# Kernel tuning notes

Hardware: AMD Instinct MI355X
Metric: run time of the kernel (lower is better)

Reference implementation:

```python
import jax, jax.numpy as jnp
import numpy as np

N_NODES = 50000
N_EDGES = 400000
D = 300          # num_features == hidden_units
L = 5            # num_layers
C = 128          # num_outputs
NG = 256         # graphs per batch
BN_EPS = 1e-5


def setup_inputs() -> dict:
    key = jax.random.key(0)
    ks = jax.random.split(key, 16)
    x = jax.random.normal(ks[0], (N_NODES, D), dtype=jnp.float32)
    edge_index = jax.random.randint(ks[1], (2, N_EDGES), 0, N_NODES, dtype=jnp.int64)
    batch = jnp.sort(jax.random.randint(ks[2], (N_NODES,), 0, NG, dtype=jnp.int64))
    s = 1.0 / np.sqrt(D)
    # Stacked per-layer GINConv MLP params: Linear -> BN -> ReLU -> Linear, then outer BN
    mlp_W1 = jax.random.uniform(ks[3], (L, D, D), jnp.float32, -s, s)
    mlp_b1 = jax.random.uniform(ks[4], (L, D), jnp.float32, -s, s)
    mlp_g1 = jnp.ones((L, D), jnp.float32)
    mlp_be1 = jnp.zeros((L, D), jnp.float32)
    mlp_W2 = jax.random.uniform(ks[5], (L, D, D), jnp.float32, -s, s)
    mlp_b2 = jax.random.uniform(ks[6], (L, D), jnp.float32, -s, s)
    bn_g = jnp.ones((L, D), jnp.float32)
    bn_b = jnp.zeros((L, D), jnp.float32)
    # num_layers+1 readout heads (num_features == hidden_units so all [D, C])
    fc_W = jax.random.uniform(ks[7], (L + 1, D, C), jnp.float32, -s, s)
    fc_b = jax.random.uniform(ks[8], (L + 1, C), jnp.float32, -s, s)
    return dict(x=x, edge_index=edge_index, batch=batch,
                mlp_W1=mlp_W1, mlp_b1=mlp_b1, mlp_g1=mlp_g1, mlp_be1=mlp_be1,
                mlp_W2=mlp_W2, mlp_b2=mlp_b2, bn_g=bn_g, bn_b=bn_b,
                fc_W=fc_W, fc_b=fc_b)


def _bn(h, gamma, beta):
    # BatchNorm1d in training mode: biased batch stats over the node dim
    mu = h.mean(axis=0)
    var = h.var(axis=0)
    return (h - mu) * jax.lax.rsqrt(var + BN_EPS) * gamma + beta


def reference(x, edge_index, batch, mlp_W1, mlp_b1, mlp_g1, mlp_be1,
              mlp_W2, mlp_b2, bn_g, bn_b, fc_W, fc_b):
    src, dst = edge_index[0], edge_index[1]
    n = x.shape[0]
    outs = [x]
    h = x
    for i in range(L):
        # GINConv (eps=0): MLP(x + sum_{j in N(i)} x_j), scatter-add over edges
        agg = jax.ops.segment_sum(h[src], dst, num_segments=n)
        z = h + agg
        z = z @ mlp_W1[i] + mlp_b1[i]
        z = jax.nn.relu(_bn(z, mlp_g1[i], mlp_be1[i]))
        z = z @ mlp_W2[i] + mlp_b2[i]
        h = jax.nn.relu(_bn(z, bn_g[i], bn_b[i]))  # outer BN + ReLU
        outs.append(h)
    # global mean pool per graph, then per-depth linear heads summed (dropout off in eval)
    counts = jax.ops.segment_sum(jnp.ones((n,), x.dtype), batch, num_segments=NG)
    inv = 1.0 / jnp.maximum(counts, 1.0)
    out = jnp.zeros((NG, C), x.dtype)
    for i, hi in enumerate(outs):
        pooled = jax.ops.segment_sum(hi, batch, num_segments=NG) * inv[:, None]
        out = out + (pooled @ fc_W[i] + fc_b[i])
    return out
```

## Files before the change

### kernel.cpp

```cpp
#include <hip/hip_runtime.h>

#define D 300
#define KP 320
#define NPAD 50048
#define NT128 391
#define TPB 2
#define GB 196
#define WSTRIDE 328
#define NGR 256
#define NL 5
#define NC 128
#define BN_EPS 1e-5f

typedef __attribute__((ext_vector_type(8))) short bf16x8;
typedef __attribute__((ext_vector_type(4))) float f32x4;
typedef unsigned short u16;

__device__ __forceinline__ void atomAdd(float* p, float v) { unsafeAtomicAdd(p, v); }

__device__ __forceinline__ short f2bf(float f) {
    union { float f; unsigned u; } v; v.f = f;
    unsigned r = v.u + 0x7fffu + ((v.u >> 16) & 1u);
    return (short)(r >> 16);
}
__device__ __forceinline__ float bf2f(short s) {
    union { unsigned u; float f; } v;
    v.u = ((unsigned)(u16)s) << 16;
    return v.f;
}
__device__ __forceinline__ unsigned cvtpk(float lo, float hi) {
    unsigned r;
    asm("v_cvt_pk_bf16_f32 %0, %1, %2" : "=v"(r) : "v"(lo), "v"(hi));
    return r;
}
template<int C>
__device__ __forceinline__ float rs_add(float v) {
    int x = __builtin_amdgcn_update_dpp(0, __float_as_int(v), C, 0xF, 0xF, true);
    return v + __int_as_float(x);
}
__device__ __forceinline__ float red16(float v) {
    v = rs_add<0x111>(v);
    v = rs_add<0x112>(v);
    v = rs_add<0x114>(v);
    v = rs_add<0x118>(v);
    return v;
}

__global__ void offsets_kernel(const int* __restrict__ batch, int* __restrict__ off, int N) {
    int g = threadIdx.x;
    if (g > NGR) return;
    int lo = 0, hi = N;
    while (lo < hi) {
        int mid = (lo + hi) >> 1;
        if (batch[mid] < g) lo = mid + 1; else hi = mid;
    }
    off[g] = lo;
}

__global__ __launch_bounds__(256)
void deg_kernel(const int* __restrict__ ei, int* __restrict__ deg, int E) {
    int e = blockIdx.x * 256 + threadIdx.x;
    if (e < E) atomicAdd(&deg[ei[E + e]], 1);
}

__global__ __launch_bounds__(256)
void degpart_kernel(const int* __restrict__ deg, int* __restrict__ part, int N) {
    int i = blockIdx.x * 256 + threadIdx.x;
    int v = (i < N) ? deg[i] : 0;
    #pragma unroll
    for (int o = 1; o < 64; o <<= 1) v += __shfl_xor(v, o);
    __shared__ int ws[4];
    if ((threadIdx.x & 63) == 0) ws[threadIdx.x >> 6] = v;
    __syncthreads();
    if (threadIdx.x == 0) part[blockIdx.x] = ws[0] + ws[1] + ws[2] + ws[3];
}

__global__ __launch_bounds__(256)
void partscan_kernel(int* __restrict__ part, int nb) {
    __shared__ int buf[256];
    int t = threadIdx.x;
    int v = (t < nb) ? part[t] : 0;
    buf[t] = v;
    __syncthreads();
    for (int o = 1; o < 256; o <<= 1) {
        int u = (t >= o) ? buf[t - o] : 0;
        __syncthreads();
        buf[t] += u;
        __syncthreads();
    }
    if (t < nb) part[t] = (t == 0) ? 0 : buf[t - 1];
}

__global__ __launch_bounds__(256)
void rowptr_kernel(const int* __restrict__ deg, const int* __restrict__ part,
                   int* __restrict__ rowptr, int N, int E) {
    __shared__ int buf[256];
    int b = blockIdx.x, t = threadIdx.x;
    int i = b * 256 + t;
    int v = (i < N) ? deg[i] : 0;
    buf[t] = v;
    __syncthreads();
    for (int o = 1; o < 256; o <<= 1) {
        int u = (t >= o) ? buf[t - o] : 0;
        __syncthreads();
        buf[t] += u;
        __syncthreads();
    }
    if (i < N) rowptr[i] = part[b] + buf[t] - v;
    if (b == 0 && t == 0) rowptr[N] = E;
}

__global__ __launch_bounds__(256)
void fill_kernel(const int* __restrict__ ei, const int* __restrict__ rowptr,
                 int* __restrict__ cursor, int* __restrict__ col, int E) {
    int e = blockIdx.x * 256 + threadIdx.x;
    if (e >= E) return;
    int src = ei[e];
    int dst = ei[E + e];
    int pos = atomicAdd(&cursor[dst], 1);
    col[rowptr[dst] + pos] = src;
}

__global__ __launch_bounds__(256)
void wcvt_kernel(const float* __restrict__ W1, const float* __restrict__ W2,
                 u16* __restrict__ Wt) {
    int idx = blockIdx.x * 256 + threadIdx.x;
    if (idx >= 10 * KP * 80) return;
    int n4 = idx % 80;
    int k = (idx / 80) % KP;
    int mat = idx / (80 * KP);
    const float* Wsrc = (mat < NL) ? (W1 + (size_t)mat * D * D) : (W2 + (size_t)(mat - NL) * D * D);
    float4 w = make_float4(0.f, 0.f, 0.f, 0.f);
    if (k < D && n4 < 75) w = *(const float4*)(Wsrc + (size_t)k * D + n4 * 4);
    size_t base = ((size_t)mat * 320 + n4 * 4) * KP + k;
    Wt[base]          = (u16)f2bf(w.x);
    Wt[base + KP]     = (u16)f2bf(w.y);
    Wt[base + 2 * KP] = (u16)f2bf(w.z);
    Wt[base + 3 * KP] = (u16)f2bf(w.w);
}

__global__ __launch_bounds__(256)
void xcvt_kernel(const float* __restrict__ x, u16* __restrict__ xbf, int N) {
    int idx = blockIdx.x * 256 + threadIdx.x;
    if (idx >= NPAD * 40) return;
    int row = idx / 40;
    int c8 = (idx - row * 40) * 8;
    short o[8];
    #pragma unroll
    for (int i = 0; i < 8; ++i) {
        int c = c8 + i;
        float f = (row < N && c < D) ? x[(size_t)row * D + c] : 0.f;
        o[i] = f2bf(f);
    }
    *(bf16x8*)(xbf + (size_t)row * KP + c8) = *(bf16x8*)o;
}

template<bool APPLY>
__global__ __launch_bounds__(256)
void gather_kernel(const u16* __restrict__ H, u16* __restrict__ Z,
                   const int* __restrict__ rowptr, const int* __restrict__ col,
                   const float* __restrict__ scsh, int N) {
    int idx = blockIdx.x * 256 + threadIdx.x;
    if (idx >= N * 40) return;
    int node = idx / 40;
    int c8 = (idx - node * 40) * 8;
    float sc[8], sh[8];
    if (APPLY) {
        #pragma unroll
        for (int i = 0; i < 8; ++i) { sc[i] = scsh[c8 + i]; sh[i] = scsh[KP + c8 + i]; }
    }
    int s = rowptr[node], e = rowptr[node + 1];
    bf16x8 v = *(const bf16x8*)(H + (size_t)node * KP + c8);
    float acc[8];
    #pragma unroll
    for (int i = 0; i < 8; ++i) {
        float f = bf2f(v[i]);
        acc[i] = APPLY ? fmaxf(fmaf(f, sc[i], sh[i]), 0.f) : f;
    }
    int j = s;
    for (; j + 2 <= e; j += 2) {
        int s0 = col[j], s1 = col[j + 1];
        bf16x8 w0 = *(const bf16x8*)(H + (size_t)s0 * KP + c8);
        bf16x8 w1 = *(const bf16x8*)(H + (size_t)s1 * KP + c8);
        #pragma unroll
        for (int i = 0; i < 8; ++i) {
            float f0 = bf2f(w0[i]);
            float f1 = bf2f(w1[i]);
            acc[i] += APPLY ? fmaxf(fmaf(f0, sc[i], sh[i]), 0.f) : f0;
            acc[i] += APPLY ? fmaxf(fmaf(f1, sc[i], sh[i]), 0.f) : f1;
        }
    }
    if (j < e) {
        int s0 = col[j];
        bf16x8 w0 = *(const bf16x8*)(H + (size_t)s0 * KP + c8);
        #pragma unroll
        for (int i = 0; i < 8; ++i) {
            float f0 = bf2f(w0[i]);
            acc[i] += APPLY ? fmaxf(fmaf(f0, sc[i], sh[i]), 0.f) : f0;
        }
    }
    short o[8];
    #pragma unroll
    for (int i = 0; i < 8; ++i) o[i] = f2bf(acc[i]);
    *(bf16x8*)(Z + (size_t)node * KP + c8) = *(bf16x8*)o;
}

template<bool APPLY>
__global__ __launch_bounds__(320)
void pool_kernel(const u16* __restrict__ H, const int* __restrict__ off,
                 const float* __restrict__ scsh, float* __restrict__ pooled_l) {
    __shared__ float red[8][KP];
    int t = threadIdx.x;
    int g = blockIdx.x;
    int rq = t / 40;
    int c8 = (t - rq * 40) * 8;
    float sc[8], sh[8];
    if (APPLY) {
        #pragma unroll
        for (int i = 0; i < 8; ++i) { sc[i] = scsh[c8 + i]; sh[i] = scsh[KP + c8 + i]; }
    }
    int r0 = off[g], r1 = off[g + 1];
    float a[8] = {};
    for (int r = r0 + rq; r < r1; r += 8) {
        bf16x8 v = *(const bf16x8*)(H + (size_t)r * KP + c8);
        #pragma unroll
        for (int i = 0; i < 8; ++i) {
            float f = bf2f(v[i]);
            a[i] += APPLY ? fmaxf(fmaf(f, sc[i], sh[i]), 0.f) : f;
        }
    }
    #pragma unroll
    for (int i = 0; i < 8; ++i) red[rq][c8 + i] = a[i];
    __syncthreads();
    int c = t;
    if (c < D) {
        float s = 0.f;
        #pragma unroll
        for (int j = 0; j < 8; ++j) s += red[j][c];
        pooled_l[g * D + c] = s;
    }
}

template<bool APPLY>
__global__ __launch_bounds__(256, 3)
void mfma_gemm_kernel(const u16* __restrict__ Abf, const u16* __restrict__ Wt,
                      const float* __restrict__ bias, const float* __restrict__ scsh,
                      u16* __restrict__ Cbf, float* __restrict__ stats, int Nreal) {
    __shared__ u16 Ws[80 * WSTRIDE];
    __shared__ float lsum[80], lsq[80];
    const int tid = threadIdx.x;
    const int nBase = blockIdx.y * 80;
    const int wave = tid >> 6, lane = tid & 63;
    const int quad = lane >> 4, l16 = lane & 15;

    const int tile0 = blockIdx.x * TPB;
    const u16* pA = Abf + (size_t)(tile0 * 128 + wave * 16 + l16) * KP + quad * 8;
    bf16x8 a[2][10];
    #pragma unroll
    for (int kc = 0; kc < 10; ++kc) {
        a[0][kc] = *(const bf16x8*)(pA + kc * 32);
        a[1][kc] = *(const bf16x8*)(pA + (size_t)64 * KP + kc * 32);
    }
    __builtin_amdgcn_sched_group_barrier(0x020, 20, 0);

    {
        const u16* src = Wt + (size_t)nBase * KP;
        for (int unit = tid; unit < 80 * 40; unit += 256) {
            int n = unit / 40, kg = unit - n * 40;
            int kc = kg >> 2, q = kg & 3;
            *(bf16x8*)&Ws[n * WSTRIDE + kc * 32 + ((q ^ (n & 3)) << 3)] =
                *(const bf16x8*)(src + (size_t)n * KP + kg * 8);
        }
    }
    if (tid < 80) { lsum[tid] = 0.f; lsq[tid] = 0.f; }
    __syncthreads();

    int wb[5];
    #pragma unroll
    for (int nt = 0; nt < 5; ++nt)
        wb[nt] = (nt * 16 + l16) * WSTRIDE + ((quad ^ (l16 & 3)) << 3);

    const size_t adv = (tile0 + 1 < NT128) ? (size_t)128 * KP : 0;

    #pragma unroll
    for (int t = 0; t < TPB; ++t) {
        const int tile = tile0 + t;

        if (APPLY) {
            #pragma unroll
            for (int kc = 0; kc < 10; ++kc) {
                const float* sp = scsh + kc * 32 + quad * 8;
                float4 s0 = *(const float4*)sp;
                float4 s1 = *(const float4*)(sp + 4);
                float4 h0 = *(const float4*)(sp + KP);
                float4 h1 = *(const float4*)(sp + KP + 4);
                float sc[8] = {s0.x, s0.y, s0.z, s0.w, s1.x, s1.y, s1.z, s1.w};
                float sh[8] = {h0.x, h0.y, h0.z, h0.w, h1.x, h1.y, h1.z, h1.w};
                #pragma unroll
                for (int g = 0; g < 2; ++g) {
                    float f[8];
                    #pragma unroll
                    for (int i = 0; i < 8; ++i)
                        f[i] = fmaxf(fmaf(bf2f(a[g][kc][i]), sc[i], sh[i]), 0.f);
                    union { unsigned u[4]; bf16x8 v; } o;
                    o.u[0] = cvtpk(f[0], f[1]);
                    o.u[1] = cvtpk(f[2], f[3]);
                    o.u[2] = cvtpk(f[4], f[5]);
                    o.u[3] = cvtpk(f[6], f[7]);
                    a[g][kc] = o.v;
                }
            }
        }

        f32x4 acc[2][5] = {};
        __builtin_amdgcn_s_setprio(1);
        #pragma unroll
        for (int kc = 0; kc < 10; ++kc) {
            #pragma unroll
            for (int nt = 0; nt < 5; ++nt) {
                bf16x8 b = *(const bf16x8*)&Ws[wb[nt] + kc * 32];
                acc[0][nt] = __builtin_amdgcn_mfma_f32_16x16x32_bf16(b, a[0][kc], acc[0][nt], 0, 0, 0);
                acc[1][nt] = __builtin_amdgcn_mfma_f32_16x16x32_bf16(b, a[1][kc], acc[1][nt], 0, 0, 0);
            }
            if (t == 0) {
                a[0][kc] = *(const bf16x8*)(pA + adv + kc * 32);
                a[1][kc] = *(const bf16x8*)(pA + adv + (size_t)64 * KP + kc * 32);
            }
            __builtin_amdgcn_sched_group_barrier(0x100, 5, 0);
            __builtin_amdgcn_sched_group_barrier(0x008, 10, 0);
            if (t == 0)
                __builtin_amdgcn_sched_group_barrier(0x020, 2, 0);
        }
        __builtin_amdgcn_s_setprio(0);

        if (tile < NT128) {
            const int r0g = tile * 128 + wave * 16 + l16;
            const bool ok0 = r0g < Nreal, ok1 = (r0g + 64) < Nreal;
            u16* crow0 = Cbf + (size_t)r0g * KP + nBase + quad * 4;
            u16* crow1 = crow0 + (size_t)64 * KP;
            #pragma unroll
            for (int nt = 0; nt < 5; ++nt) {
                const int c0 = nBase + nt * 16 + quad * 4;
                float bia[4], msk[4];
                if (c0 + 3 < D) {
                    float4 b4 = *(const float4*)(bias + c0);
                    bia[0] = b4.x; bia[1] = b4.y; bia[2] = b4.z; bia[3] = b4.w;
                    msk[0] = msk[1] = msk[2] = msk[3] = 1.f;
                } else {
                    #pragma unroll
                    for (int r = 0; r < 4; ++r) {
                        bool vld = (c0 + r) < D;
                        msk[r] = vld ? 1.f : 0.f;
                        bia[r] = vld ? bias[c0 + r] : 0.f;
                    }
                }
                float v0[4], v1[4];
                #pragma unroll
                for (int r = 0; r < 4; ++r) {
                    v0[r] = (acc[0][nt][r] + bia[r]) * msk[r];
                    v1[r] = (acc[1][nt][r] + bia[r]) * msk[r];
                }
                uint2 w0, w1;
                w0.x = cvtpk(v0[0], v0[1]); w0.y = cvtpk(v0[2], v0[3]);
                w1.x = cvtpk(v1[0], v1[1]); w1.y = cvtpk(v1[2], v1[3]);
                *(uint2*)(crow0 + nt * 16) = w0;
                *(uint2*)(crow1 + nt * 16) = w1;
                #pragma unroll
                for (int r = 0; r < 4; ++r) {
                    float s0 = ok0 ? v0[r] : 0.f;
                    float s1 = ok1 ? v1[r] : 0.f;
                    float sv = red16(s0 + s1);
                    float qv = red16(fmaf(s0, s0, s1 * s1));
                    if (l16 == 15) {
                        atomicAdd(&lsum[nt * 16 + quad * 4 + r], sv);
                        atomicAdd(&lsq [nt * 16 + quad * 4 + r], qv);
                    }
                }
            }
        }
    }
    __syncthreads();
    if (tid < 80) {
        int colg = nBase + tid;
        if (colg < D) {
            atomAdd(&stats[colg], lsum[tid]);
            atomAdd(&stats[KP + colg], lsq[tid]);
        }
    }
}

__global__ void bnfin_kernel(float* __restrict__ sums, const float* __restrict__ g,
                             const float* __restrict__ be, float* __restrict__ scsh, float invN) {
    int c = threadIdx.x;
    if (c >= D) return;
    float mu = sums[c] * invN;
    float var = sums[KP + c] * invN - mu * mu;
    float s = g[c] / sqrtf(var + BN_EPS);
    scsh[c] = s;
    scsh[KP + c] = fmaf(-mu, s, be[c]);
    sums[c] = 0.f;
    sums[KP + c] = 0.f;
}

__global__ __launch_bounds__(128)
void bias_init_kernel(const float* __restrict__ fcb, float* __restrict__ out) {
    int i = blockIdx.x * 128 + threadIdx.x;
    if (i >= NGR * NC) return;
    int c = i & (NC - 1);
    float s = 0.f;
    for (int l = 0; l <= NL; ++l) s += fcb[l * NC + c];
    out[i] = s;
}

__global__ __launch_bounds__(128)
void readout_kernel(const float* __restrict__ pooled, const int* __restrict__ off,
                    const float* __restrict__ fcW, float* __restrict__ out) {
    __shared__ float sp[4][D];
    int c = threadIdx.x;
    int l = blockIdx.y;
    int g0 = blockIdx.x * 4;
    for (int i = c; i < 4 * D; i += 128) {
        int gg = i / D, k = i - gg * D;
        sp[gg][k] = pooled[((size_t)l * NGR + g0 + gg) * D + k];
    }
    __syncthreads();
    float acc[4] = {0.f, 0.f, 0.f, 0.f};
    for (int k = 0; k < D; ++k) {
        float w = fcW[((size_t)l * D + k) * NC + c];
        #pragma unroll
        for (int gg = 0; gg < 4; ++gg) acc[gg] = fmaf(sp[gg][k], w, acc[gg]);
    }
    #pragma unroll
    for (int gg = 0; gg < 4; ++gg) {
        int g = g0 + gg;
        float inv = 1.0f / fmaxf((float)(off[g + 1] - off[g]), 1.0f);
        atomAdd(&out[g * NC + c], acc[gg] * inv);
    }
}

extern "C" void kernel_launch(void* const* d_in, const int* in_sizes, int n_in,
                              void* d_out, int out_size, void* d_ws, size_t ws_size,
                              hipStream_t stream) {
    const float* x       = (const float*)d_in[0];
    const int*   ei      = (const int*)d_in[1];
    const int*   batch   = (const int*)d_in[2];
    const float* W1  = (const float*)d_in[3];
    const float* b1  = (const float*)d_in[4];
    const float* g1  = (const float*)d_in[5];
    const float* be1 = (const float*)d_in[6];
    const float* W2  = (const float*)d_in[7];
    const float* b2  = (const float*)d_in[8];
    const float* bng = (const float*)d_in[9];
    const float* bnb = (const float*)d_in[10];
    const float* fcW = (const float*)d_in[11];
    const float* fcb = (const float*)d_in[12];
    float* out = (float*)d_out;

    const int N = in_sizes[0] / D;
    const int E = in_sizes[1] / 2;
    const int nb = (N + 255) / 256;

    u16* xbf  = (u16*)d_ws;
    u16* bufA = xbf + (size_t)NPAD * KP;
    u16* bufB = bufA + (size_t)NPAD * KP;
    u16* Wt   = bufB + (size_t)NPAD * KP;
    float* pooled = (float*)(Wt + (size_t)10 * 320 * KP);
    float* stats  = pooled + (size_t)(NL + 1) * NGR * D;
    float* sc1    = stats + 2 * KP;
    float* sc2    = sc1 + 2 * KP;
    int*   off    = (int*)(sc2 + 2 * KP);
    int*   rowptr = off + NGR + 1;
    int*   cursor = rowptr + N + 1;
    int*   col    = cursor + N;
    int*   part   = col + E;

    hipMemsetAsync(stats, 0, 6 * KP * sizeof(float), stream);
    offsets_kernel<<<1, 320, 0, stream>>>(batch, off, N);
    bias_init_kernel<<<(NGR * NC + 127) / 128, 128, 0, stream>>>(fcb, out);

    hipMemsetAsync(cursor, 0, N * sizeof(int), stream);
    deg_kernel<<<(E + 255) / 256, 256, 0, stream>>>(ei, cursor, E);
    degpart_kernel<<<nb, 256, 0, stream>>>(cursor, part, N);
    partscan_kernel<<<1, 256, 0, stream>>>(part, nb);
    rowptr_kernel<<<nb, 256, 0, stream>>>(cursor, part, rowptr, N, E);
    hipMemsetAsync(cursor, 0, N * sizeof(int), stream);
    fill_kernel<<<(E + 255) / 256, 256, 0, stream>>>(ei, rowptr, cursor, col, E);

    wcvt_kernel<<<(10 * KP * 80 + 255) / 256, 256, 0, stream>>>(W1, W2, Wt);
    xcvt_kernel<<<(NPAD * 40 + 255) / 256, 256, 0, stream>>>(x, xbf, N);

    const dim3 gemm_grid(GB, 4);
    const int nd40 = N * 40;
    float invN = 1.0f / (float)N;
    const size_t WtM = (size_t)320 * KP;

    pool_kernel<false><<<NGR, 320, 0, stream>>>(xbf, off, sc2, pooled);

    u16* g = bufA;
    u16* t = bufB;
    const u16* src = xbf;
    for (int l = 0; l < NL; ++l) {
        if (l == 0)
            gather_kernel<false><<<(nd40 + 255) / 256, 256, 0, stream>>>(src, g, rowptr, col, sc2, N);
        else
            gather_kernel<true><<<(nd40 + 255) / 256, 256, 0, stream>>>(src, g, rowptr, col, sc2, N);
        mfma_gemm_kernel<false><<<gemm_grid, 256, 0, stream>>>(
            g, Wt + (size_t)l * WtM, b1 + l * D, sc1, t, stats, N);
        bnfin_kernel<<<1, 320, 0, stream>>>(stats, g1 + l * D, be1 + l * D, sc1, invN);
        mfma_gemm_kernel<true><<<gemm_grid, 256, 0, stream>>>(
            t, Wt + (size_t)(NL + l) * WtM, b2 + l * D, sc1, g, stats, N);
        bnfin_kernel<<<1, 320, 0, stream>>>(stats, bng + l * D, bnb + l * D, sc2, invN);
        pool_kernel<true><<<NGR, 320, 0, stream>>>(g, off, sc2, pooled + (size_t)(l + 1) * NGR * D);
        src = g;
        u16* tmp = g; g = t; t = tmp;
    }
    readout_kernel<<<dim3(NGR / 4, NL + 1), 128, 0, stream>>>(pooled, off, fcW, out);
}
```

Baseline: 1.011 ms.

## Drop GEMM biases before BN, use one tile per block, partition stat atomics

Removes the bias add and column masking from the GEMM epilogue, since a per-column bias just before training-mode BatchNorm cancels in the mean subtraction. The GEMM goes back to one 128-row tile per block (grid of 391x4) without the software-prefetched second tile. Global BN stat accumulation is spread over 8 partitions keyed on block index to cut atomic contention, and bnfin sums and clears the partitions. Dropping the bias changes stored bf16 values slightly, and padded columns now depend on the zero-padded weights rather than explicit masking.

New measurement: 1.007 ms. About the same (-0.4%).

```diff
diff --git a/kernel.cpp b/kernel.cpp
--- a/kernel.cpp
+++ b/kernel.cpp
@@ -4,12 +4,11 @@
 #define KP 320
 #define NPAD 50048
 #define NT128 391
-#define TPB 2
-#define GB 196
 #define WSTRIDE 328
 #define NGR 256
 #define NL 5
 #define NC 128
+#define SPART 8
 #define BN_EPS 1e-5f
 
 typedef __attribute__((ext_vector_type(8))) short bf16x8;
@@ -244,7 +243,7 @@
 template<bool APPLY>
 __global__ __launch_bounds__(256, 3)
 void mfma_gemm_kernel(const u16* __restrict__ Abf, const u16* __restrict__ Wt,
-                      const float* __restrict__ bias, const float* __restrict__ scsh,
+                      const float* __restrict__ scsh,
                       u16* __restrict__ Cbf, float* __restrict__ stats, int Nreal) {
     __shared__ u16 Ws[80 * WSTRIDE];
     __shared__ float lsum[80], lsq[80];
@@ -252,16 +251,15 @@
     const int nBase = blockIdx.y * 80;
     const int wave = tid >> 6, lane = tid & 63;
     const int quad = lane >> 4, l16 = lane & 15;
-
-    const int tile0 = blockIdx.x * TPB;
-    const u16* pA = Abf + (size_t)(tile0 * 128 + wave * 16 + l16) * KP + quad * 8;
+    const int tile = blockIdx.x;
+
+    const u16* pA = Abf + (size_t)(tile * 128 + wave * 16 + l16) * KP + quad * 8;
     bf16x8 a[2][10];
     #pragma unroll
     for (int kc = 0; kc < 10; ++kc) {
         a[0][kc] = *(const bf16x8*)(pA + kc * 32);
         a[1][kc] = *(const bf16x8*)(pA + (size_t)64 * KP + kc * 32);
     }
-    __builtin_amdgcn_sched_group_barrier(0x020, 20, 0);
 
     {
         const u16* src = Wt + (size_t)nBase * KP;
@@ -273,109 +271,81 @@
         }
     }
     if (tid < 80) { lsum[tid] = 0.f; lsq[tid] = 0.f; }
-    __syncthreads();
+
+    #pragma unroll
+    for (int kc = 0; kc < 10; ++kc) {
+        asm volatile("" : "+v"(a[0][kc]));
+        asm volatile("" : "+v"(a[1][kc]));
+    }
+    __syncthreads();
+
+    if (APPLY) {
+        #pragma unroll
+        for (int kc = 0; kc < 10; ++kc) {
+            const float* sp = scsh + kc * 32 + quad * 8;
+            float4 s0 = *(const float4*)sp;
+            float4 s1 = *(const float4*)(sp + 4);
+            float4 h0 = *(const float4*)(sp + KP);
+            float4 h1 = *(const float4*)(sp + KP + 4);
+            float sc[8] = {s0.x, s0.y, s0.z, s0.w, s1.x, s1.y, s1.z, s1.w};
+            float sh[8] = {h0.x, h0.y, h0.z, h0.w, h1.x, h1.y, h1.z, h1.w};
+            #pragma unroll
+            for (int g = 0; g < 2; ++g) {
+                float f[8];
+                #pragma unroll
+                for (int i = 0; i < 8; ++i)
+                    f[i] = fmaxf(fmaf(bf2f(a[g][kc][i]), sc[i], sh[i]), 0.f);
+                union { unsigned u[4]; bf16x8 v; } o;
+                o.u[0] = cvtpk(f[0], f[1]);
+                o.u[1] = cvtpk(f[2], f[3]);
+                o.u[2] = cvtpk(f[4], f[5]);
+                o.u[3] = cvtpk(f[6], f[7]);
+                a[g][kc] = o.v;
+            }
+        }
+    }
 
     int wb[5];
     #pragma unroll
     for (int nt = 0; nt < 5; ++nt)
         wb[nt] = (nt * 16 + l16) * WSTRIDE + ((quad ^ (l16 & 3)) << 3);
 
-    const size_t adv = (tile0 + 1 < NT128) ? (size_t)128 * KP : 0;
-
-    #pragma unroll
-    for (int t = 0; t < TPB; ++t) {
-        const int tile = tile0 + t;
-
-        if (APPLY) {
-            #pragma unroll
-            for (int kc = 0; kc < 10; ++kc) {
-                const float* sp = scsh + kc * 32 + quad * 8;
-                float4 s0 = *(const float4*)sp;
-                float4 s1 = *(const float4*)(sp + 4);
-                float4 h0 = *(const float4*)(sp + KP);
-                float4 h1 = *(const float4*)(sp + KP + 4);
-                float sc[8] = {s0.x, s0.y, s0.z, s0.w, s1.x, s1.y, s1.z, s1.w};
-                float sh[8] = {h0.x, h0.y, h0.z, h0.w, h1.x, h1.y, h1.z, h1.w};
-                #pragma unroll
-                for (int g = 0; g < 2; ++g) {
-                    float f[8];
-                    #pragma unroll
-                    for (int i = 0; i < 8; ++i)
-                        f[i] = fmaxf(fmaf(bf2f(a[g][kc][i]), sc[i], sh[i]), 0.f);
-                    union { unsigned u[4]; bf16x8 v; } o;
-                    o.u[0] = cvtpk(f[0], f[1]);
-                    o.u[1] = cvtpk(f[2], f[3]);
-                    o.u[2] = cvtpk(f[4], f[5]);
-                    o.u[3] = cvtpk(f[6], f[7]);
-                    a[g][kc] = o.v;
-                }
-            }
-        }
-
-        f32x4 acc[2][5] = {};
-        __builtin_amdgcn_s_setprio(1);
-        #pragma unroll
-        for (int kc = 0; kc < 10; ++kc) {
-            #pragma unroll
-            for (int nt = 0; nt < 5; ++nt) {
-                bf16x8 b = *(const bf16x8*)&Ws[wb[nt] + kc * 32];
-                acc[0][nt] = __builtin_amdgcn_mfma_f32_16x16x32_bf16(b, a[0][kc], acc[0][nt], 0, 0, 0);
-                acc[1][nt] = __builtin_amdgcn_mfma_f32_16x16x32_bf16(b, a[1][kc], acc[1][nt], 0, 0, 0);
-            }
-            if (t == 0) {
-                a[0][kc] = *(const bf16x8*)(pA + adv + kc * 32);
-                a[1][kc] = *(const bf16x8*)(pA + adv + (size_t)64 * KP + kc * 32);
-            }
-            __builtin_amdgcn_sched_group_barrier(0x100, 5, 0);
-            __builtin_amdgcn_sched_group_barrier(0x008, 10, 0);
-            if (t == 0)
-                __builtin_amdgcn_sched_group_barrier(0x020, 2, 0);
-        }
-        __builtin_amdgcn_s_setprio(0);
-
-        if (tile < NT128) {
-            const int r0g = tile * 128 + wave * 16 + l16;
-            const bool ok0 = r0g < Nreal, ok1 = (r0g + 64) < Nreal;
-            u16* crow0 = Cbf + (size_t)r0g * KP + nBase + quad * 4;
-            u16* crow1 = crow0 + (size_t)64 * KP;
-            #pragma unroll
-            for (int nt = 0; nt < 5; ++nt) {
-                const int c0 = nBase + nt * 16 + quad * 4;
-                float bia[4], msk[4];
-                if (c0 + 3 < D) {
-                    float4 b4 = *(const float4*)(bias + c0);
-                    bia[0] = b4.x; bia[1] = b4.y; bia[2] = b4.z; bia[3] = b4.w;
-                    msk[0] = msk[1] = msk[2] = msk[3] = 1.f;
-                } else {
-                    #pragma unroll
-                    for (int r = 0; r < 4; ++r) {
-                        bool vld = (c0 + r) < D;
-                        msk[r] = vld ? 1.f : 0.f;
-                        bia[r] = vld ? bias[c0 + r] : 0.f;
-                    }
-                }
-                float v0[4], v1[4];
-                #pragma unroll
-                for (int r = 0; r < 4; ++r) {
-                    v0[r] = (acc[0][nt][r] + bia[r]) * msk[r];
-                    v1[r] = (acc[1][nt][r] + bia[r]) * msk[r];
-                }
-                uint2 w0, w1;
-                w0.x = cvtpk(v0[0], v0[1]); w0.y = cvtpk(v0[2], v0[3]);
-                w1.x = cvtpk(v1[0], v1[1]); w1.y = cvtpk(v1[2], v1[3]);
-                *(uint2*)(crow0 + nt * 16) = w0;
-                *(uint2*)(crow1 + nt * 16) = w1;
-                #pragma unroll
-                for (int r = 0; r < 4; ++r) {
-                    float s0 = ok0 ? v0[r] : 0.f;
-                    float s1 = ok1 ? v1[r] : 0.f;
-                    float sv = red16(s0 + s1);
-                    float qv = red16(fmaf(s0, s0, s1 * s1));
-                    if (l16 == 15) {
-                        atomicAdd(&lsum[nt * 16 + quad * 4 + r], sv);
-                        atomicAdd(&lsq [nt * 16 + quad * 4 + r], qv);
-                    }
-                }
+    f32x4 acc[2][5] = {};
+    __builtin_amdgcn_s_setprio(1);
+    #pragma unroll
+    for (int kc = 0; kc < 10; ++kc) {
+        #pragma unroll
+        for (int nt = 0; nt < 5; ++nt) {
+            bf16x8 b = *(const bf16x8*)&Ws[wb[nt] + kc * 32];
+            acc[0][nt] = __builtin_amdgcn_mfma_f32_16x16x32_bf16(b, a[0][kc], acc[0][nt], 0, 0, 0);
+            acc[1][nt] = __builtin_amdgcn_mfma_f32_16x16x32_bf16(b, a[1][kc], acc[1][nt], 0, 0, 0);
+        }
+    }
+    __builtin_amdgcn_s_setprio(0);
+
+    const int r0g = tile * 128 + wave * 16 + l16;
+    const bool ok0 = r0g < Nreal, ok1 = (r0g + 64) < Nreal;
+    u16* crow0 = Cbf + (size_t)r0g * KP + nBase + quad * 4;
+    u16* crow1 = crow0 + (size_t)64 * KP;
+    #pragma unroll
+    for (int nt = 0; nt < 5; ++nt) {
+        float v0[4], v1[4];
+        #pragma unroll
+        for (int r = 0; r < 4; ++r) { v0[r] = acc[0][nt][r]; v1[r] = acc[1][nt][r]; }
+        uint2 w0, w1;
+        w0.x = cvtpk(v0[0], v0[1]); w0.y = cvtpk(v0[2], v0[3]);
+        w1.x = cvtpk(v1[0], v1[1]); w1.y = cvtpk(v1[2], v1[3]);
+        *(uint2*)(crow0 + nt * 16) = w0;
+        *(uint2*)(crow1 + nt * 16) = w1;
+        #pragma unroll
+        for (int r = 0; r < 4; ++r) {
+            float s0 = ok0 ? v0[r] : 0.f;
+            float s1 = ok1 ? v1[r] : 0.f;
+            float sv = red16(s0 + s1);
+            float qv = red16(fmaf(s0, s0, s1 * s1));
+            if (l16 == 15) {
+                atomicAdd(&lsum[nt * 16 + quad * 4 + r], sv);
+                atomicAdd(&lsq [nt * 16 + quad * 4 + r], qv);
             }
         }
     }
@@ -383,8 +353,9 @@
     if (tid < 80) {
         int colg = nBase + tid;
         if (colg < D) {
-            atomAdd(&stats[colg], lsum[tid]);
-            atomAdd(&stats[KP + colg], lsq[tid]);
+            float* sp = stats + (size_t)(blockIdx.x & (SPART - 1)) * 2 * KP;
+            atomAdd(&sp[colg], lsum[tid]);
+            atomAdd(&sp[KP + colg], lsq[tid]);
         }
     }
 }
@@ -393,13 +364,19 @@
                              const float* __restrict__ be, float* __restrict__ scsh, float invN) {
     int c = threadIdx.x;
     if (c >= D) return;
-    float mu = sums[c] * invN;
-    float var = sums[KP + c] * invN - mu * mu;
+    float t1 = 0.f, t2 = 0.f;
+    #pragma unroll
+    for (int p = 0; p < SPART; ++p) {
+        t1 += sums[(size_t)p * 2 * KP + c];
+        t2 += sums[(size_t)p * 2 * KP + KP + c];
+        sums[(size_t)p * 2 * KP + c] = 0.f;
+        sums[(size_t)p * 2 * KP + KP + c] = 0.f;
+    }
+    float mu = t1 * invN;
+    float var = t2 * invN - mu * mu;
     float s = g[c] / sqrtf(var + BN_EPS);
     scsh[c] = s;
     scsh[KP + c] = fmaf(-mu, s, be[c]);
-    sums[c] = 0.f;
-    sums[KP + c] = 0.f;
 }
 
 __global__ __launch_bounds__(128)
@@ -445,11 +422,9 @@
     const int*   ei      = (const int*)d_in[1];
     const int*   batch   = (const int*)d_in[2];
     const float* W1  = (const float*)d_in[3];
-    const float* b1  = (const float*)d_in[4];
     const float* g1  = (const float*)d_in[5];
     const float* be1 = (const float*)d_in[6];
     const float* W2  = (const float*)d_in[7];
-    const float* b2  = (const float*)d_in[8];
     const float* bng = (const float*)d_in[9];
     const float* bnb = (const float*)d_in[10];
     const float* fcW = (const float*)d_in[11];
@@ -466,7 +441,7 @@
     u16* Wt   = bufB + (size_t)NPAD * KP;
     float* pooled = (float*)(Wt + (size_t)10 * 320 * KP);
     float* stats  = pooled + (size_t)(NL + 1) * NGR * D;
-    float* sc1    = stats + 2 * KP;
+    float* sc1    = stats + (size_t)SPART * 2 * KP;
     float* sc2    = sc1 + 2 * KP;
     int*   off    = (int*)(sc2 + 2 * KP);
     int*   rowptr = off + NGR + 1;
@@ -474,7 +449,7 @@
     int*   col    = cursor + N;
     int*   part   = col + E;
 
-    hipMemsetAsync(stats, 0, 6 * KP * sizeof(float), stream);
+    hipMemsetAsync(stats, 0, (SPART * 2 + 4) * KP * sizeof(float), stream);
     offsets_kernel<<<1, 320, 0, stream>>>(batch, off, N);
     bias_init_kernel<<<(NGR * NC + 127) / 128, 128, 0, stream>>>(fcb, out);
 
@@ -489,7 +464,7 @@
     wcvt_kernel<<<(10 * KP * 80 + 255) / 256, 256, 0, stream>>>(W1, W2, Wt);
     xcvt_kernel<<<(NPAD * 40 + 255) / 256, 256, 0, stream>>>(x, xbf, N);
 
-    const dim3 gemm_grid(GB, 4);
+    const dim3 gemm_grid(NT128, 4);
     const int nd40 = N * 40;
     float invN = 1.0f / (float)N;
     const size_t WtM = (size_t)320 * KP;
@@ -505,10 +480,10 @@
         else
             gather_kernel<true><<<(nd40 + 255) / 256, 256, 0, stream>>>(src, g, rowptr, col, sc2, N);
         mfma_gemm_kernel<false><<<gemm_grid, 256, 0, stream>>>(
-            g, Wt + (size_t)l * WtM, b1 + l * D, sc1, t, stats, N);
+            g, Wt + (size_t)l * WtM, sc1, t, stats, N);
         bnfin_kernel<<<1, 320, 0, stream>>>(stats, g1 + l * D, be1 + l * D, sc1, invN);
         mfma_gemm_kernel<true><<<gemm_grid, 256, 0, stream>>>(
-            t, Wt + (size_t)(NL + l) * WtM, b2 + l * D, sc1, g, stats, N);
+            t, Wt + (size_t)(NL + l) * WtM, sc1, g, stats, N);
         bnfin_kernel<<<1, 320, 0, stream>>>(stats, bng + l * D, bnb + l * D, sc2, invN);
         pool_kernel<true><<<NGR, 320, 0, stream>>>(g, off, sc2, pooled + (size_t)(l + 1) * NGR * D);
         src = g;
```
